# Kernel tuning notes

Hardware: AMD Instinct MI355X
Metric: run time of the kernel (lower is better)

Reference implementation:

```python
import jax, jax.numpy as jnp
import numpy as np

D_MODEL = 256
NUM_HEADS = 4
D_HEAD = D_MODEL // NUM_HEADS
LN_EPS = 1e-5
NEG_INF = -1e9


def setup_inputs() -> dict:
    key = jax.random.key(0)
    ks = jax.random.split(key, 8)
    B, N = 4, 2048
    s = 1.0 / np.sqrt(D_MODEL)
    return {
        "x": jax.random.normal(ks[0], (B, N, D_MODEL), dtype=jnp.float32),
        "Wq": jax.random.normal(ks[1], (D_MODEL, D_MODEL), dtype=jnp.float32) * s,
        "Wk": jax.random.normal(ks[2], (D_MODEL, D_MODEL), dtype=jnp.float32) * s,
        "Wv": jax.random.normal(ks[3], (D_MODEL, D_MODEL), dtype=jnp.float32) * s,
        "Wo": jax.random.normal(ks[4], (D_MODEL, D_MODEL), dtype=jnp.float32) * s,
        "bo": jnp.zeros((D_MODEL,), dtype=jnp.float32),
        "gamma": jnp.ones((D_MODEL,), dtype=jnp.float32),
        "beta": jnp.zeros((D_MODEL,), dtype=jnp.float32),
        "k_neighbors": 8,
    }


def build_knn_adj(x, k):
    # x: [B, N, D]; returns symmetric 0/1 adjacency [B, N, N]
    B, N, _ = x.shape
    xn = x / jnp.maximum(jnp.linalg.norm(x, axis=-1, keepdims=True), 1e-12)
    sim = jnp.einsum('bnd,bmd->bnm', xn, xn)  # [B, N, N]
    _, idx = jax.lax.top_k(sim, k + 1)        # [B, N, k+1]
    b = jnp.arange(B)[:, None, None]
    r = jnp.arange(N)[None, :, None]
    adj = jnp.zeros((B, N, N), dtype=jnp.float32).at[b, r, idx].add(1.0)
    adj = jnp.maximum(adj, jnp.swapaxes(adj, 1, 2))
    return adj


def layer_norm(x, gamma, beta):
    mu = jnp.mean(x, axis=-1, keepdims=True)
    var = jnp.mean(jnp.square(x - mu), axis=-1, keepdims=True)
    return (x - mu) * jax.lax.rsqrt(var + LN_EPS) * gamma + beta


def reference(x, Wq, Wk, Wv, Wo, bo, gamma, beta, k_neighbors):
    B, N, D = x.shape
    adj = build_knn_adj(x, k_neighbors)  # [B, N, N]

    def split_heads(t):  # [B, N, D] -> [B, H, N, d]
        return jnp.transpose(t.reshape(B, N, NUM_HEADS, D_HEAD), (0, 2, 1, 3))

    q = split_heads(x @ Wq)
    k = split_heads(x @ Wk)
    v = split_heads(x @ Wv)

    scores = jnp.einsum('bhnd,bhmd->bhnm', q, k) / jnp.sqrt(jnp.float32(D_HEAD))
    scores = jnp.where(adj[:, None, :, :] > 0, scores, NEG_INF)
    attn = jax.nn.softmax(scores, axis=-1)  # dropout is identity at inference
    out = jnp.einsum('bhnm,bhmd->bhnd', attn, v)
    out = jnp.transpose(out, (0, 2, 1, 3)).reshape(B, N, D)
    out = out @ Wo + bo
    return layer_norm(x + out, gamma, beta)
```

## Files before the change

### kernel.cpp

```cpp
#include <hip/hip_runtime.h>
#include <hip/hip_bf16.h>
#include <math.h>

#define BATCH 4
#define N 2048
#define D 256
#define NH 4
#define DH 64
#define TOPK 9
#define NEG_BIG -1e30f

typedef __bf16 bf16;
typedef __bf16 bf16x8 __attribute__((ext_vector_type(8)));
typedef float f32x4 __attribute__((ext_vector_type(4)));

#define PK3(a,b,c) ((a) | ((b) << 2) | ((c) << 4))
#define PK6(a,b,c,d,e,f) ((a) | ((b) << 2) | ((c) << 4) | ((d) << 6) | ((e) << 8) | ((f) << 10))

#define WAITVM(Nc) __builtin_amdgcn_s_waitcnt((((Nc) & 0xf)) | (7u << 4) | (0xfu << 8) | ((((unsigned)(Nc)) >> 4) << 14))

__device__ __forceinline__ void async_cp16(const bf16* g, const bf16* l) {
  __builtin_amdgcn_global_load_lds(
      (const __attribute__((address_space(1))) void*)(uintptr_t)g,
      (__attribute__((address_space(3))) void*)(uintptr_t)l, 16, 0, 0);
}

__global__ __launch_bounds__(64) void prep_xn_w_kernel(const float* __restrict__ x,
                                                       const float* __restrict__ Wq,
                                                       const float* __restrict__ Wk,
                                                       const float* __restrict__ Wv,
                                                       const float* __restrict__ Wo,
                                                       bf16* __restrict__ XsN,
                                                       bf16* __restrict__ Wt,
                                                       uint4* __restrict__ mask4) {
  int blk = blockIdx.x;
  int lane = threadIdx.x;
  if (blk < 8192) {
    float4 v = *(const float4*)(x + (size_t)blk * D + lane * 4);
    float ss = v.x * v.x + v.y * v.y + v.z * v.z + v.w * v.w;
    for (int off = 32; off; off >>= 1) ss += __shfl_down(ss, off);
    ss = __shfl(ss, 0);
    float sc = 1.0f / fmaxf(sqrtf(ss), 1e-12f);
    float xs[4] = {v.x * sc, v.y * sc, v.z * sc, v.w * sc};
    bf16* o = XsN + (size_t)blk * 768 + lane * 4;
#pragma unroll
    for (int j = 0; j < 4; ++j) {
      float xv = xs[j];
      bf16 h = (bf16)xv;
      float r1 = xv - (float)h;
      bf16 m = (bf16)r1;
      o[j] = h;
      o[256 + j] = m;
      o[512 + j] = (bf16)(r1 - (float)m);
    }
  } else if (blk < 9216) {
    int jj = blk - 8192;
    const float* W = (jj < 256) ? Wq : (jj < 512) ? Wk : (jj < 768) ? Wv : Wo;
    int j = jj & 255;
    bf16* dst = Wt + (size_t)jj * 512;
    for (int k = lane; k < 256; k += 64) {
      float w = W[(size_t)k * D + j];
      bf16 h = (bf16)w;
      dst[k] = h;
      dst[256 + k] = (bf16)(w - (float)h);
    }
  } else {
    int base = (blk - 9216) * 1024 + lane;
#pragma unroll
    for (int t = 0; t < 16; ++t)
      mask4[base + t * 64] = make_uint4(0, 0, 0, 0);
  }
}

__global__ __launch_bounds__(64) void prep_raw_kernel(const float* __restrict__ x,
                                                      bf16* __restrict__ XsRaw) {
  int row = blockIdx.x;
  int lane = threadIdx.x;
  float4 v = *(const float4*)(x + (size_t)row * D + lane * 4);
  float xs[4] = {v.x, v.y, v.z, v.w};
  bf16* o = XsRaw + (size_t)row * 512 + lane * 4;
#pragma unroll
  for (int j = 0; j < 4; ++j) {
    bf16 h = (bf16)xs[j];
    o[j] = h;
    o[256 + j] = (bf16)(xs[j] - (float)h);
  }
}

__global__ __launch_bounds__(256) void gemm_bt_kernel(const bf16* __restrict__ A,
                                                      const bf16* __restrict__ B,
                                                      float* __restrict__ C,
                                                      int lda, int ldb, int ldc,
                                                      int nsteps, int amap, int bmap,
                                                      long sA, long sB, long sC,
                                                      int mode) {
  __shared__ bf16 As[2][128 * 64];
  __shared__ bf16 Bs[2][128 * 64];
  int tid = threadIdx.x;
  int lane = tid & 63;
  int wv = tid >> 6;
  int wm = (wv >> 1) * 64;
  int wn = (wv & 1) * 64;
  int bx, by, z;
  if (mode) {
    int g = blockIdx.x;
    int xcd = g & 7;
    int slot = g >> 3;
    z = xcd >> 1;
    int t = (xcd & 1) * 68 + slot;
    by = 0;
    while (t >= 16 - by) { t -= 16 - by; ++by; }
    bx = by + t;
  } else {
    bx = blockIdx.x;
    by = blockIdx.y;
    z = blockIdx.z;
  }
  int row0 = by * 128;
  int col0 = bx * 128;
  const bf16* Ab = A + (size_t)z * sA + (size_t)row0 * lda;
  const bf16* Bb = B + (size_t)z * sB + (size_t)col0 * ldb;
  float* Cb = C + (size_t)z * sC;

  int rbase = tid >> 3;
  int gperm = (tid & 7) ^ (rbase & 7);
  const bf16* ga0 = Ab + (size_t)rbase * lda + gperm * 8;
  const bf16* gb0 = Bb + (size_t)rbase * ldb + gperm * 8;
  int ldsoff = tid * 8;

  int fr = lane & 15;
  int fq = (lane >> 4) * 8;

  f32x4 acc[4][4] = {};

  auto issue = [&](int st, int buf) {
    int ch = st >> 2;
    int aoff = (((amap >> (ch * 2)) & 3) << 8) | ((st & 3) << 6);
    int boff = (((bmap >> (ch * 2)) & 3) << 8) | ((st & 3) << 6);
#pragma unroll
    for (int q = 0; q < 4; ++q)
      async_cp16(ga0 + (size_t)q * 32 * lda + aoff, &As[buf][ldsoff + q * 2048]);
#pragma unroll
    for (int q = 0; q < 4; ++q)
      async_cp16(gb0 + (size_t)q * 32 * ldb + boff, &Bs[buf][ldsoff + q * 2048]);
  };

  issue(0, 0);
  for (int st = 0; st < nsteps; ++st) {
    int buf = st & 1;
    if (st + 1 < nsteps) {
      issue(st + 1, buf ^ 1);
      WAITVM(8);
    } else {
      WAITVM(0);
    }
    __builtin_amdgcn_s_barrier();
#pragma unroll
    for (int ks = 0; ks < 64; ks += 32) {
      bf16x8 af[4], bfr[4];
#pragma unroll
      for (int mi = 0; mi < 4; ++mi) {
        int r = wm + mi * 16 + fr;
        int G = (ks + fq) >> 3;
        af[mi] = *(const bf16x8*)&As[buf][r * 64 + ((G ^ (r & 7)) << 3)];
      }
#pragma unroll
      for (int nj = 0; nj < 4; ++nj) {
        int r = wn + nj * 16 + fr;
        int G = (ks + fq) >> 3;
        bfr[nj] = *(const bf16x8*)&Bs[buf][r * 64 + ((G ^ (r & 7)) << 3)];
      }
#pragma unroll
      for (int mi = 0; mi < 4; ++mi)
#pragma unroll
        for (int nj = 0; nj < 4; ++nj)
          acc[mi][nj] = __builtin_amdgcn_mfma_f32_16x16x32_bf16(af[mi], bfr[nj], acc[mi][nj], 0, 0, 0);
    }
    __builtin_amdgcn_s_barrier();
  }

  int er = (lane >> 4) * 4;
  int ec = lane & 15;
#pragma unroll
  for (int mi = 0; mi < 4; ++mi)
#pragma unroll
    for (int nj = 0; nj < 4; ++nj) {
      int rb = row0 + wm + mi * 16 + er;
      int cb = col0 + wn + nj * 16 + ec;
      if (mode) {
#pragma unroll
        for (int reg = 0; reg < 4; ++reg)
          __builtin_nontemporal_store(acc[mi][nj][reg],
                                      &Cb[(size_t)(rb + reg) * ldc + cb]);
        if (bx != by) {
#pragma unroll
          for (int reg = 0; reg < 4; ++reg)
            __builtin_nontemporal_store(acc[mi][nj][reg],
                                        &Cb[(size_t)cb * ldc + rb + reg]);
        }
      } else {
#pragma unroll
        for (int reg = 0; reg < 4; ++reg)
          Cb[(size_t)(rb + reg) * ldc + cb] = acc[mi][nj][reg];
      }
    }
}

__global__ __launch_bounds__(64) void topk_adj_kernel(const float* __restrict__ sim,
                                                      unsigned* __restrict__ mask) {
  int row = blockIdx.x;
  int lane = threadIdx.x;
  int b = row >> 11, r = row & 2047;
  const float* srow = sim + (size_t)row * N;
  float v[32];
#pragma unroll
  for (int it = 0; it < 8; ++it) {
    float4 q = *(const float4*)(srow + it * 256 + lane * 4);
    v[it * 4 + 0] = q.x; v[it * 4 + 1] = q.y;
    v[it * 4 + 2] = q.z; v[it * 4 + 3] = q.w;
  }
  unsigned removed = 0;
  for (int rs = 0; rs < TOPK; ++rs) {
    float m = -3e38f;
    int mi = 0;
#pragma unroll
    for (int i = 0; i < 32; ++i) {
      float vv = ((removed >> i) & 1u) ? -3e38f : v[i];
      if (vv > m) { m = vv; mi = i; }
    }
    int gidx = ((mi >> 2) << 8) + lane * 4 + (mi & 3);
    for (int off = 32; off; off >>= 1) {
      float om = __shfl_down(m, off);
      int og = __shfl_down(gidx, off);
      if (om > m || (om == m && og < gidx)) { m = om; gidx = og; }
    }
    gidx = __shfl(gidx, 0);
    if (((gidx >> 2) & 63) == lane)
      removed |= 1u << (((gidx >> 8) << 2) | (gidx & 3));
    if (lane == 0) {
      atomicOr(&mask[(size_t)row * 64 + (gidx >> 5)], 1u << (gidx & 31));
      atomicOr(&mask[(((size_t)b << 11) + gidx) * 64 + (r >> 5)], 1u << (r & 31));
    }
  }
}

__global__ __launch_bounds__(256) void attn_kernel(const float* __restrict__ qkv,
                                                   const unsigned* __restrict__ mask,
                                                   bf16* __restrict__ aos) {
  __shared__ float sq[4][256];
  __shared__ unsigned short nbr[4][2048];
  __shared__ int s_nn[4];
  int wv = threadIdx.x >> 6;
  int lane = threadIdx.x & 63;
  int g = blockIdx.x;
  int xcd = g & 7;
  int b = xcd >> 1;
  int tile = (xcd & 1) * 256 + (g >> 3);
  int bn = b * N + tile * 4 + wv;
  if (lane == 0) s_nn[wv] = 0;
  *(float4*)&sq[wv][lane * 4] = *(const float4*)(qkv + (size_t)bn * 768 + lane * 4);
  __syncthreads();
  unsigned bits = mask[(size_t)bn * (N / 32) + lane];
  while (bits) {
    int bit = __ffs(bits) - 1;
    bits &= bits - 1;
    int p = atomicAdd(&s_nn[wv], 1);
    nbr[wv][p] = (unsigned short)(lane * 32 + bit);
  }
  __syncthreads();
  int nn = s_nn[wv];
  const float* base = qkv + (size_t)b * N * 768;
  float acc[4] = {0.f, 0.f, 0.f, 0.f};

  auto score4 = [&](int j, float* s) {
    const float* kr = base + (size_t)j * 768 + 256;
#pragma unroll
    for (int h = 0; h < 4; ++h) {
      float a = 0.f;
#pragma unroll
      for (int c = 0; c < DH; c += 4) {
        float4 kk = *(const float4*)(kr + h * DH + c);
        a += sq[wv][h * DH + c] * kk.x + sq[wv][h * DH + c + 1] * kk.y +
             sq[wv][h * DH + c + 2] * kk.z + sq[wv][h * DH + c + 3] * kk.w;
      }
      s[h] = a * 0.125f;
    }
  };

  if (nn <= 64) {
    float s[4] = {NEG_BIG, NEG_BIG, NEG_BIG, NEG_BIG};
    if (lane < nn) score4(nbr[wv][lane], s);
    float w[4], l[4];
#pragma unroll
    for (int h = 0; h < 4; ++h) {
      float m = s[h];
      for (int off = 32; off; off >>= 1) m = fmaxf(m, __shfl_down(m, off));
      m = __shfl(m, 0);
      float e = (lane < nn) ? __expf(s[h] - m) : 0.f;
      float ls = e;
      for (int off = 32; off; off >>= 1) ls += __shfl_down(ls, off);
      l[h] = __shfl(ls, 0);
      w[h] = e;
    }
    int i = 0;
    for (; i + 4 <= nn; i += 4) {
      int j0 = nbr[wv][i + 0], j1 = nbr[wv][i + 1];
      int j2 = nbr[wv][i + 2], j3 = nbr[wv][i + 3];
      const float* p0 = base + (size_t)j0 * 768 + 512;
      const float* p1 = base + (size_t)j1 * 768 + 512;
      const float* p2 = base + (size_t)j2 * 768 + 512;
      const float* p3 = base + (size_t)j3 * 768 + 512;
#pragma unroll
      for (int h = 0; h < 4; ++h) {
        acc[h] += __shfl(w[h], i + 0) * p0[h * DH + lane] +
                  __shfl(w[h], i + 1) * p1[h * DH + lane] +
                  __shfl(w[h], i + 2) * p2[h * DH + lane] +
                  __shfl(w[h], i + 3) * p3[h * DH + lane];
      }
    }
    for (; i < nn; ++i) {
      const float* p0 = base + (size_t)nbr[wv][i] * 768 + 512;
#pragma unroll
      for (int h = 0; h < 4; ++h) acc[h] += __shfl(w[h], i) * p0[h * DH + lane];
    }
#pragma unroll
    for (int h = 0; h < 4; ++h) acc[h] /= l[h];
  } else {
    float m[4] = {NEG_BIG, NEG_BIG, NEG_BIG, NEG_BIG};
    for (int i0 = 0; i0 < nn; i0 += 64) {
      float s[4] = {NEG_BIG, NEG_BIG, NEG_BIG, NEG_BIG};
      if (i0 + lane < nn) score4(nbr[wv][i0 + lane], s);
#pragma unroll
      for (int h = 0; h < 4; ++h) m[h] = fmaxf(m[h], s[h]);
    }
#pragma unroll
    for (int h = 0; h < 4; ++h) {
      for (int off = 32; off; off >>= 1) m[h] = fmaxf(m[h], __shfl_down(m[h], off));
      m[h] = __shfl(m[h], 0);
    }
    float l[4] = {0.f, 0.f, 0.f, 0.f};
    for (int i0 = 0; i0 < nn; i0 += 64) {
      float s[4] = {NEG_BIG, NEG_BIG, NEG_BIG, NEG_BIG};
      if (i0 + lane < nn) score4(nbr[wv][i0 + lane], s);
      float e[4];
#pragma unroll
      for (int h = 0; h < 4; ++h) {
        e[h] = (i0 + lane < nn) ? __expf(s[h] - m[h]) : 0.f;
        float ls = e[h];
        for (int off = 32; off; off >>= 1) ls += __shfl_down(ls, off);
        l[h] += __shfl(ls, 0);
      }
      int lim = min(64, nn - i0);
      for (int ii = 0; ii < lim; ++ii) {
        const float* p0 = base + (size_t)nbr[wv][i0 + ii] * 768 + 512;
#pragma unroll
        for (int h = 0; h < 4; ++h) acc[h] += __shfl(e[h], ii) * p0[h * DH + lane];
      }
    }
#pragma unroll
    for (int h = 0; h < 4; ++h) acc[h] /= l[h];
  }
#pragma unroll
  for (int h = 0; h < 4; ++h) {
    float a = acc[h];
    bf16 hi = (bf16)a;
    aos[(size_t)bn * 512 + h * DH + lane] = hi;
    aos[(size_t)bn * 512 + 256 + h * DH + lane] = (bf16)(a - (float)hi);
  }
}

__global__ __launch_bounds__(64) void ln_kernel(const float* __restrict__ x,
                                                const float* __restrict__ proj,
                                                const float* __restrict__ bo,
                                                const float* __restrict__ gamma,
                                                const float* __restrict__ beta,
                                                float* __restrict__ out) {
  int row = blockIdx.x;
  int lane = threadIdx.x;
  size_t base = (size_t)row * D + lane * 4;
  float4 xv = *(const float4*)(x + base);
  float4 pv = *(const float4*)(proj + base);
  float4 bv = *(const float4*)(bo + lane * 4);
  float u0 = xv.x + pv.x + bv.x, u1 = xv.y + pv.y + bv.y;
  float u2 = xv.z + pv.z + bv.z, u3 = xv.w + pv.w + bv.w;
  float s = u0 + u1 + u2 + u3;
  for (int off = 32; off; off >>= 1) s += __shfl_down(s, off);
  s = __shfl(s, 0);
  float mean = s * (1.0f / D);
  float d0 = u0 - mean, d1 = u1 - mean, d2 = u2 - mean, d3 = u3 - mean;
  float ss = d0 * d0 + d1 * d1 + d2 * d2 + d3 * d3;
  for (int off = 32; off; off >>= 1) ss += __shfl_down(ss, off);
  ss = __shfl(ss, 0);
  float rstd = rsqrtf(ss * (1.0f / D) + 1e-5f);
  float4 gv = *(const float4*)(gamma + lane * 4);
  float4 be = *(const float4*)(beta + lane * 4);
  float4 o;
  o.x = d0 * rstd * gv.x + be.x;
  o.y = d1 * rstd * gv.y + be.y;
  o.z = d2 * rstd * gv.z + be.z;
  o.w = d3 * rstd * gv.w + be.w;
  *(float4*)(out + base) = o;
}

extern "C" void kernel_launch(void* const* d_in, const int* in_sizes, int n_in,
                              void* d_out, int out_size, void* d_ws, size_t ws_size,
                              hipStream_t stream) {
  const float* x     = (const float*)d_in[0];
  const float* Wq    = (const float*)d_in[1];
  const float* Wk    = (const float*)d_in[2];
  const float* Wv    = (const float*)d_in[3];
  const float* Wo    = (const float*)d_in[4];
  const float* bo    = (const float*)d_in[5];
  const float* gamma = (const float*)d_in[6];
  const float* beta  = (const float*)d_in[7];
  float* out = (float*)d_out;

  char* ws = (char*)d_ws;
  bf16* XsN      = (bf16*)(ws);
  float* sim     = (float*)(ws + 12582912);
  unsigned* mask = (unsigned*)(ws + 79986688);
  bf16* Wt       = (bf16*)(ws + 82083840);
  bf16* XsRaw    = (bf16*)(ws);
  float* qkv     = (float*)(ws + 8388608);
  bf16* aos      = (bf16*)(ws + 33554432);
  float* proj    = (float*)(ws + 41943040);

  const int AMAP_SIM = PK6(0, 0, 1, 0, 0, 0);
  const int BMAP_SIM = PK6(0, 1, 0, 0, 0, 0);
  const int AMAP_2T  = PK3(0, 1, 0);
  const int BMAP_2T  = PK3(0, 0, 1);

  prep_xn_w_kernel<<<9344, 64, 0, stream>>>(x, Wq, Wk, Wv, Wo, XsN, Wt,
                                            (uint4*)mask);

  gemm_bt_kernel<<<dim3(544, 1, 1), 256, 0, stream>>>(
      XsN, XsN, sim, 768, 768, N, 12, AMAP_SIM, BMAP_SIM,
      (long)N * 768, (long)N * 768, (long)N * N, 1);
  topk_adj_kernel<<<BATCH * N, 64, 0, stream>>>(sim, mask);

  prep_raw_kernel<<<BATCH * N, 64, 0, stream>>>(x, XsRaw);
  gemm_bt_kernel<<<dim3(6, 64, 1), 256, 0, stream>>>(
      XsRaw, Wt, qkv, 512, 512, 768, 8, AMAP_2T, BMAP_2T, 0, 0, 0, 0);

  attn_kernel<<<(BATCH * N) / 4, 256, 0, stream>>>(qkv, mask, aos);

  gemm_bt_kernel<<<dim3(2, 64, 1), 256, 0, stream>>>(
      aos, Wt + (size_t)768 * 512, proj, 512, 512, D, 8, AMAP_2T, BMAP_2T, 0, 0, 0, 0);
  ln_kernel<<<BATCH * N, 64, 0, stream>>>(x, proj, bo, gamma, beta, out);
}
```

Measured before the change: 205.1 us.

## Reuse normalized split-bf16 x for QKV GEMM and fuse it with sim GEMM launch

Drops the separate raw-x split kernel. The QKV projection now reads the already-normalized split-bf16 x and multiplies each output row by its saved norm in the epilogue. When the workspace is large enough, the similarity GEMM tiles and the QKV GEMM tiles run in one combined launch, so both GEMMs fill the device together and one kernel launch goes away. The trade-offs are slightly different rounding, since the QKV inputs come from normalized values, and a workspace-size-dependent code path.

```diff
diff --git a/kernel.cpp b/kernel.cpp
--- a/kernel.cpp
+++ b/kernel.cpp
@@ -25,14 +25,15 @@
       (__attribute__((address_space(3))) void*)(uintptr_t)l, 16, 0, 0);
 }
 
-__global__ __launch_bounds__(64) void prep_xn_w_kernel(const float* __restrict__ x,
-                                                       const float* __restrict__ Wq,
-                                                       const float* __restrict__ Wk,
-                                                       const float* __restrict__ Wv,
-                                                       const float* __restrict__ Wo,
-                                                       bf16* __restrict__ XsN,
-                                                       bf16* __restrict__ Wt,
-                                                       uint4* __restrict__ mask4) {
+__global__ __launch_bounds__(64) void prep_kernel(const float* __restrict__ x,
+                                                  const float* __restrict__ Wq,
+                                                  const float* __restrict__ Wk,
+                                                  const float* __restrict__ Wv,
+                                                  const float* __restrict__ Wo,
+                                                  bf16* __restrict__ XsN,
+                                                  bf16* __restrict__ Wt,
+                                                  float* __restrict__ norms,
+                                                  uint4* __restrict__ mask4) {
   int blk = blockIdx.x;
   int lane = threadIdx.x;
   if (blk < 8192) {
@@ -40,7 +41,9 @@
     float ss = v.x * v.x + v.y * v.y + v.z * v.z + v.w * v.w;
     for (int off = 32; off; off >>= 1) ss += __shfl_down(ss, off);
     ss = __shfl(ss, 0);
-    float sc = 1.0f / fmaxf(sqrtf(ss), 1e-12f);
+    float nrm = fmaxf(sqrtf(ss), 1e-12f);
+    if (lane == 0) norms[blk] = nrm;
+    float sc = 1.0f / nrm;
     float xs[4] = {v.x * sc, v.y * sc, v.z * sc, v.w * sc};
     bf16* o = XsN + (size_t)blk * 768 + lane * 4;
 #pragma unroll
@@ -72,55 +75,20 @@
   }
 }
 
-__global__ __launch_bounds__(64) void prep_raw_kernel(const float* __restrict__ x,
-                                                      bf16* __restrict__ XsRaw) {
-  int row = blockIdx.x;
-  int lane = threadIdx.x;
-  float4 v = *(const float4*)(x + (size_t)row * D + lane * 4);
-  float xs[4] = {v.x, v.y, v.z, v.w};
-  bf16* o = XsRaw + (size_t)row * 512 + lane * 4;
-#pragma unroll
-  for (int j = 0; j < 4; ++j) {
-    bf16 h = (bf16)xs[j];
-    o[j] = h;
-    o[256 + j] = (bf16)(xs[j] - (float)h);
-  }
-}
-
-__global__ __launch_bounds__(256) void gemm_bt_kernel(const bf16* __restrict__ A,
-                                                      const bf16* __restrict__ B,
-                                                      float* __restrict__ C,
-                                                      int lda, int ldb, int ldc,
-                                                      int nsteps, int amap, int bmap,
-                                                      long sA, long sB, long sC,
-                                                      int mode) {
-  __shared__ bf16 As[2][128 * 64];
-  __shared__ bf16 Bs[2][128 * 64];
+__device__ __forceinline__ void gemm_core(bf16* As, bf16* Bs,
+                                          const bf16* __restrict__ Ab,
+                                          const bf16* __restrict__ Bb,
+                                          float* __restrict__ Cb,
+                                          int lda, int ldb, int ldc,
+                                          int nsteps, int amap, int bmap,
+                                          int row0, int col0,
+                                          bool mirror, bool nt,
+                                          const float* __restrict__ rowscale) {
   int tid = threadIdx.x;
   int lane = tid & 63;
   int wv = tid >> 6;
   int wm = (wv >> 1) * 64;
   int wn = (wv & 1) * 64;
-  int bx, by, z;
-  if (mode) {
-    int g = blockIdx.x;
-    int xcd = g & 7;
-    int slot = g >> 3;
-    z = xcd >> 1;
-    int t = (xcd & 1) * 68 + slot;
-    by = 0;
-    while (t >= 16 - by) { t -= 16 - by; ++by; }
-    bx = by + t;
-  } else {
-    bx = blockIdx.x;
-    by = blockIdx.y;
-    z = blockIdx.z;
-  }
-  int row0 = by * 128;
-  int col0 = bx * 128;
-  const bf16* Ab = A + (size_t)z * sA + (size_t)row0 * lda;
-  const bf16* Bb = B + (size_t)z * sB + (size_t)col0 * ldb;
-  float* Cb = C + (size_t)z * sC;
 
   int rbase = tid >> 3;
   int gperm = (tid & 7) ^ (rbase & 7);
@@ -139,10 +107,10 @@
     int boff = (((bmap >> (ch * 2)) & 3) << 8) | ((st & 3) << 6);
 #pragma unroll
     for (int q = 0; q < 4; ++q)
-      async_cp16(ga0 + (size_t)q * 32 * lda + aoff, &As[buf][ldsoff + q * 2048]);
+      async_cp16(ga0 + (size_t)q * 32 * lda + aoff, &As[buf * 8192 + ldsoff + q * 2048]);
 #pragma unroll
     for (int q = 0; q < 4; ++q)
-      async_cp16(gb0 + (size_t)q * 32 * ldb + boff, &Bs[buf][ldsoff + q * 2048]);
+      async_cp16(gb0 + (size_t)q * 32 * ldb + boff, &Bs[buf * 8192 + ldsoff + q * 2048]);
   };
 
   issue(0, 0);
@@ -162,13 +130,13 @@
       for (int mi = 0; mi < 4; ++mi) {
         int r = wm + mi * 16 + fr;
         int G = (ks + fq) >> 3;
-        af[mi] = *(const bf16x8*)&As[buf][r * 64 + ((G ^ (r & 7)) << 3)];
+        af[mi] = *(const bf16x8*)&As[buf * 8192 + r * 64 + ((G ^ (r & 7)) << 3)];
       }
 #pragma unroll
       for (int nj = 0; nj < 4; ++nj) {
         int r = wn + nj * 16 + fr;
         int G = (ks + fq) >> 3;
-        bfr[nj] = *(const bf16x8*)&Bs[buf][r * 64 + ((G ^ (r & 7)) << 3)];
+        bfr[nj] = *(const bf16x8*)&Bs[buf * 8192 + r * 64 + ((G ^ (r & 7)) << 3)];
       }
 #pragma unroll
       for (int mi = 0; mi < 4; ++mi)
@@ -182,17 +150,22 @@
   int er = (lane >> 4) * 4;
   int ec = lane & 15;
 #pragma unroll
-  for (int mi = 0; mi < 4; ++mi)
+  for (int mi = 0; mi < 4; ++mi) {
+    int rb = row0 + wm + mi * 16 + er;
+    float scl[4] = {1.f, 1.f, 1.f, 1.f};
+    if (rowscale) {
+      float4 s4 = *(const float4*)(rowscale + rb);
+      scl[0] = s4.x; scl[1] = s4.y; scl[2] = s4.z; scl[3] = s4.w;
+    }
 #pragma unroll
     for (int nj = 0; nj < 4; ++nj) {
-      int rb = row0 + wm + mi * 16 + er;
       int cb = col0 + wn + nj * 16 + ec;
-      if (mode) {
+      if (nt) {
 #pragma unroll
         for (int reg = 0; reg < 4; ++reg)
           __builtin_nontemporal_store(acc[mi][nj][reg],
                                       &Cb[(size_t)(rb + reg) * ldc + cb]);
-        if (bx != by) {
+        if (mirror) {
 #pragma unroll
           for (int reg = 0; reg < 4; ++reg)
             __builtin_nontemporal_store(acc[mi][nj][reg],
@@ -201,9 +174,82 @@
       } else {
 #pragma unroll
         for (int reg = 0; reg < 4; ++reg)
-          Cb[(size_t)(rb + reg) * ldc + cb] = acc[mi][nj][reg];
-      }
-    }
+          Cb[(size_t)(rb + reg) * ldc + cb] = acc[mi][nj][reg] * scl[reg];
+      }
+    }
+  }
+}
+
+__global__ __launch_bounds__(256) void gemm_sim_kernel(const bf16* __restrict__ XsN,
+                                                       float* __restrict__ sim,
+                                                       int amap, int bmap) {
+  __shared__ bf16 As[2 * 128 * 64];
+  __shared__ bf16 Bs[2 * 128 * 64];
+  int g = blockIdx.x;
+  int xcd = g & 7;
+  int slot = g >> 3;
+  int z = xcd >> 1;
+  int t = (xcd & 1) * 68 + slot;
+  int by = 0;
+  while (t >= 16 - by) { t -= 16 - by; ++by; }
+  int bx = by + t;
+  gemm_core(As, Bs,
+            XsN + (size_t)z * N * 768 + (size_t)by * 128 * 768,
+            XsN + (size_t)z * N * 768 + (size_t)bx * 128 * 768,
+            sim + (size_t)z * N * N,
+            768, 768, N, 12, amap, bmap, by * 128, bx * 128,
+            bx != by, true, nullptr);
+}
+
+__global__ __launch_bounds__(256) void gemm_gen_kernel(const bf16* __restrict__ A,
+                                                       const bf16* __restrict__ B,
+                                                       float* __restrict__ C,
+                                                       int lda, int ldb, int ldc,
+                                                       int nsteps, int amap, int bmap,
+                                                       const float* __restrict__ rowscale) {
+  __shared__ bf16 As[2 * 128 * 64];
+  __shared__ bf16 Bs[2 * 128 * 64];
+  gemm_core(As, Bs,
+            A + (size_t)blockIdx.y * 128 * lda,
+            B + (size_t)blockIdx.x * 128 * ldb,
+            C, lda, ldb, ldc, nsteps, amap, bmap,
+            blockIdx.y * 128, blockIdx.x * 128, false, false, rowscale);
+}
+
+__global__ __launch_bounds__(256) void gemm_fused_kernel(const bf16* __restrict__ XsN,
+                                                         float* __restrict__ sim,
+                                                         int amap_s, int bmap_s,
+                                                         const bf16* __restrict__ Wt,
+                                                         float* __restrict__ qkv,
+                                                         int amap_q, int bmap_q,
+                                                         const float* __restrict__ norms) {
+  __shared__ bf16 As[2 * 128 * 64];
+  __shared__ bf16 Bs[2 * 128 * 64];
+  int g = blockIdx.x;
+  if (g < 544) {
+    int xcd = g & 7;
+    int slot = g >> 3;
+    int z = xcd >> 1;
+    int t = (xcd & 1) * 68 + slot;
+    int by = 0;
+    while (t >= 16 - by) { t -= 16 - by; ++by; }
+    int bx = by + t;
+    gemm_core(As, Bs,
+              XsN + (size_t)z * N * 768 + (size_t)by * 128 * 768,
+              XsN + (size_t)z * N * 768 + (size_t)bx * 128 * 768,
+              sim + (size_t)z * N * N,
+              768, 768, N, 12, amap_s, bmap_s, by * 128, bx * 128,
+              bx != by, true, nullptr);
+  } else {
+    int t = g - 544;
+    int bx = t % 6;
+    int by = t / 6;
+    gemm_core(As, Bs,
+              XsN + (size_t)by * 128 * 768,
+              Wt + (size_t)bx * 128 * 512,
+              qkv, 768, 512, 768, 8, amap_q, bmap_q,
+              by * 128, bx * 128, false, false, norms);
+  }
 }
 
 __global__ __launch_bounds__(64) void topk_adj_kernel(const float* __restrict__ sim,
@@ -418,33 +464,37 @@
   char* ws = (char*)d_ws;
   bf16* XsN      = (bf16*)(ws);
   float* sim     = (float*)(ws + 12582912);
+  float* norms   = (float*)(ws + 79691776);
   unsigned* mask = (unsigned*)(ws + 79986688);
   bf16* Wt       = (bf16*)(ws + 82083840);
-  bf16* XsRaw    = (bf16*)(ws);
-  float* qkv     = (float*)(ws + 8388608);
-  bf16* aos      = (bf16*)(ws + 33554432);
-  float* proj    = (float*)(ws + 41943040);
+
+  bool big = ws_size >= (size_t)125075456;
+  float* qkv  = (float*)(ws + (big ? 83132416  : 12582912));
+  bf16* aos   = (bf16*)(ws + (big ? 108298240 : 37748736));
+  float* proj = (float*)(ws + (big ? 116686848 : 46137344));
 
   const int AMAP_SIM = PK6(0, 0, 1, 0, 0, 0);
   const int BMAP_SIM = PK6(0, 1, 0, 0, 0, 0);
   const int AMAP_2T  = PK3(0, 1, 0);
   const int BMAP_2T  = PK3(0, 0, 1);
 
-  prep_xn_w_kernel<<<9344, 64, 0, stream>>>(x, Wq, Wk, Wv, Wo, XsN, Wt,
-                                            (uint4*)mask);
-
-  gemm_bt_kernel<<<dim3(544, 1, 1), 256, 0, stream>>>(
-      XsN, XsN, sim, 768, 768, N, 12, AMAP_SIM, BMAP_SIM,
-      (long)N * 768, (long)N * 768, (long)N * N, 1);
-  topk_adj_kernel<<<BATCH * N, 64, 0, stream>>>(sim, mask);
-
-  prep_raw_kernel<<<BATCH * N, 64, 0, stream>>>(x, XsRaw);
-  gemm_bt_kernel<<<dim3(6, 64, 1), 256, 0, stream>>>(
-      XsRaw, Wt, qkv, 512, 512, 768, 8, AMAP_2T, BMAP_2T, 0, 0, 0, 0);
+  prep_kernel<<<9344, 64, 0, stream>>>(x, Wq, Wk, Wv, Wo, XsN, Wt, norms,
+                                       (uint4*)mask);
+
+  if (big) {
+    gemm_fused_kernel<<<928, 256, 0, stream>>>(
+        XsN, sim, AMAP_SIM, BMAP_SIM, Wt, qkv, AMAP_2T, BMAP_2T, norms);
+    topk_adj_kernel<<<BATCH * N, 64, 0, stream>>>(sim, mask);
+  } else {
+    gemm_sim_kernel<<<544, 256, 0, stream>>>(XsN, sim, AMAP_SIM, BMAP_SIM);
+    topk_adj_kernel<<<BATCH * N, 64, 0, stream>>>(sim, mask);
+    gemm_gen_kernel<<<dim3(6, 64), 256, 0, stream>>>(
+        XsN, Wt, qkv, 768, 512, 768, 8, AMAP_2T, BMAP_2T, norms);
+  }
 
   attn_kernel<<<(BATCH * N) / 4, 256, 0, stream>>>(qkv, mask, aos);
 
-  gemm_bt_kernel<<<dim3(2, 64, 1), 256, 0, stream>>>(
-      aos, Wt + (size_t)768 * 512, proj, 512, 512, D, 8, AMAP_2T, BMAP_2T, 0, 0, 0, 0);
+  gemm_gen_kernel<<<dim3(2, 64), 256, 0, stream>>>(
+      aos, Wt + (size_t)768 * 512, proj, 512, 512, D, 8, AMAP_2T, BMAP_2T, nullptr);
   ln_kernel<<<BATCH * N, 64, 0, stream>>>(x, proj, bo, gamma, beta, out);
 }
```

Result: faster. 198.7 us (-3.1%).
